# Performance work log

Measured on AMD Instinct MI355X. Metric: run time of the kernel, lower is better.

Reference implementation:

```python
import jax, jax.numpy as jnp
import numpy as np

BETA = 1.0  # lagr_softmax default inverse temperature

def setup_inputs() -> dict:
    key = jax.random.key(0)
    ks = jax.random.split(key, 5)
    B, Tq, Tk, Eq, Ek, E, H = 2, 2048, 2048, 1024, 1024, 1024, 16
    s = lambda d: 1.0 / np.sqrt(d)
    return {
        "gq": jax.random.normal(ks[0], (B, Tq, Eq), jnp.float32),
        "gk": jax.random.normal(ks[1], (B, Tk, Ek), jnp.float32),
        "WQ": jax.random.normal(ks[2], (E, Eq), jnp.float32) * s(Eq),
        "WK": jax.random.normal(ks[3], (E, Ek), jnp.float32) * s(Ek),
        "Wmix": jax.random.normal(ks[4], (1, H), jnp.float32) * s(H),
    }

def reference(gq, gk, WQ, WK, Wmix):
    B, Tq, _ = gq.shape
    H = Wmix.shape[1]
    E = WQ.shape[0]
    D = E // H
    # Linear projections (bias=False): x @ W.T
    q = (gq @ WQ.T).reshape(B, Tq, H, D)          # (B,Tq,H,D)
    k = (gk @ WK.T).reshape(B, -1, H, D)          # (B,Tk,H,D)
    # scores q @ k^T per head: (B,H,Tq,Tk)
    a = jnp.einsum('bqhd,bkhd->bhqk', q, k)
    # mix_heads: Linear(n_heads -> 1) applied over head axis
    a = jnp.einsum('bhqk,h->bqk', a, Wmix[0])     # (B,Tq,Tk)
    # lagr_softmax: (1/beta) * logsumexp(beta * a, dim=-1)
    out = jax.nn.logsumexp(BETA * a, axis=-1) / BETA  # (B,Tq)
    return out[:, None, :]                        # (B,1,Tq) matching torch shape
```

## Files before the change

### kernel.cpp

```cpp
#include <hip/hip_runtime.h>
#include <hip/hip_bf16.h>
#include <math.h>

#define B_    2
#define TQ    2048
#define TK    2048
#define E_    1024
#define MTOT  4096

typedef __attribute__((ext_vector_type(8))) short bf16x8;
typedef __attribute__((ext_vector_type(4))) float f32x4;

__device__ __forceinline__ unsigned short f2bf(float x) {
  unsigned int u = __float_as_uint(x);
  u += 0x7fff + ((u >> 16) & 1);
  return (unsigned short)(u >> 16);
}

__device__ __forceinline__ void load_lds16(const void* g, void* l) {
  __builtin_amdgcn_global_load_lds(
      (const __attribute__((address_space(1))) unsigned int*)g,
      (__attribute__((address_space(3))) unsigned int*)l, 16, 0, 0);
}

#define BARRIER() do { asm volatile("" ::: "memory"); __builtin_amdgcn_s_barrier(); asm volatile("" ::: "memory"); } while (0)
#define WAIT_VM6()   asm volatile("s_waitcnt vmcnt(6)" ::: "memory")
#define WAIT_VM0()   asm volatile("s_waitcnt vmcnt(0)" ::: "memory")


__device__ __forceinline__ void stage_A(const unsigned short* gsrc, unsigned short* lds,
                                        int tid, int kt) {
  const int r  = tid >> 3;
  const int c8 = ((tid & 7) ^ (r & 7)) * 8;
  const unsigned short* g = gsrc + (size_t)r * E_ + (size_t)kt * 64 + c8;
  unsigned short* l = lds + tid * 8;
#pragma unroll
  for (int i = 0; i < 4; ++i)
    load_lds16(g + (size_t)(64 * i) * E_, l + 4096 * i);
}
__device__ __forceinline__ void stage_B(const unsigned short* gsrc, unsigned short* lds,
                                        int tid, int kt) {
  const int r  = tid >> 3;
  const int c8 = ((tid & 7) ^ (r & 7)) * 8;
  const unsigned short* g = gsrc + (size_t)r * E_ + (size_t)kt * 64 + c8;
  unsigned short* l = lds + tid * 8;
#pragma unroll
  for (int i = 0; i < 2; ++i)
    load_lds16(g + (size_t)(64 * i) * E_, l + 4096 * i);
}

#define LDS_AT(base, row, o) ((const bf16x8*)((base) + (((row) * 128 + ((o) ^ (((row) & 7) << 4))) >> 1)))

#define READ_A_ALL()                                                          \
  do {                                                                        \
    _Pragma("unroll") for (int f = 0; f < 4; ++f)                             \
      _Pragma("unroll") for (int ks = 0; ks < 2; ++ks)                        \
        a[f][ks] = *LDS_AT(Ac, wm * 64 + f * 16 + li16, ks * 64 + hi4 * 16);  \
  } while (0)

#define READ_B(g0)                                                            \
  do {                                                                        \
    _Pragma("unroll") for (int g = (g0); g < (g0) + 2; ++g)                   \
      _Pragma("unroll") for (int ks = 0; ks < 2; ++ks)                        \
        b[g][ks] = *LDS_AT(Bc, wn * 64 + g * 16 + li16, ks * 64 + hi4 * 16);  \
  } while (0)

#define MFMA_HALF(g0)                                                         \
  do {                                                                        \
    __builtin_amdgcn_s_setprio(1);                                            \
    _Pragma("unroll") for (int ks = 0; ks < 2; ++ks)                          \
      _Pragma("unroll") for (int f = 0; f < 4; ++f)                           \
        _Pragma("unroll") for (int g = (g0); g < (g0) + 2; ++g)               \
          acc[f][g] = __builtin_amdgcn_mfma_f32_16x16x32_bf16(                \
              a[f][ks], b[g][ks], acc[f][g], 0, 0, 0);                        \
    __builtin_amdgcn_s_setprio(0);                                            \
  } while (0)

#define GEMM_PIPELINE()                                                       \
  do {                                                                        \
    stage_B(Bg, Bsl[0], tid, 0); stage_A(Ag, Asl[0], tid, 0);                 \
    stage_B(Bg, Bsl[1], tid, 1); stage_A(Ag, Asl[1], tid, 1);                 \
    WAIT_VM6();                   \
    int s0 = 0, s2 = 2;                                     \
    for (int t = 0; t < 16; ++t) {                                            \
      BARRIER();                                                              \
      const unsigned short* Ac = Asl[s0];                                     \
      const unsigned short* Bc = Bsl[s0];                                     \
                                                         \
      READ_A_ALL(); READ_B(0);                                                \
      stage_B(Bg, Bsl[s2], tid, (t + 2) & 15);                                \
      MFMA_HALF(0);                                                           \
                                                        \
      READ_B(2);                                                              \
      stage_A(Ag, Asl[s2], tid, (t + 2) & 15);                                \
      MFMA_HALF(2);                                                           \
      WAIT_VM6();                                                             \
      s0 = (s0 == 2) ? 0 : s0 + 1;                                            \
      s2 = (s2 == 2) ? 0 : s2 + 1;                                            \
    }                                                                         \
  } while (0)

__global__ void prep_kernel(const float* __restrict__ gq, const float* __restrict__ gk,
                            const float* __restrict__ WQ, const float* __restrict__ WK,
                            const float* __restrict__ Wmix,
                            unsigned short* __restrict__ gqb, unsigned short* __restrict__ gkb,
                            unsigned short* __restrict__ wqb, unsigned short* __restrict__ wkb) {
  const int NGQ = (B_ * TQ * E_) / 4;
  const int NW  = (E_ * E_) / 4;
  const int total = 2 * NGQ + 2 * NW;
  for (int idx = blockIdx.x * blockDim.x + threadIdx.x; idx < total;
       idx += gridDim.x * blockDim.x) {
    const float4* src; unsigned short* dst; int local; float scale = 1.0f;
    if (idx < NGQ)            { src = (const float4*)gq; dst = gqb; local = idx; }
    else if (idx < 2 * NGQ)   { src = (const float4*)gk; dst = gkb; local = idx - NGQ; }
    else if (idx < 2*NGQ+NW)  { src = (const float4*)WQ; dst = wqb; local = idx - 2*NGQ;
                                scale = Wmix[local >> 14]; }
    else                      { src = (const float4*)WK; dst = wkb; local = idx - 2*NGQ - NW; }
    float4 v = src[local];
    ushort4 o;
    o.x = f2bf(v.x * scale); o.y = f2bf(v.y * scale);
    o.z = f2bf(v.z * scale); o.w = f2bf(v.w * scale);
    ((ushort4*)dst)[local] = o;
  }
}

__global__ __launch_bounds__(512, 2) void proj_kernel(
    const unsigned short* __restrict__ gqb, const unsigned short* __restrict__ gkb,
    const unsigned short* __restrict__ wqb, const unsigned short* __restrict__ wkb,
    unsigned short* __restrict__ qp, unsigned short* __restrict__ kp) {
  __shared__ __align__(16) unsigned short Asl[3][16384];
  __shared__ __align__(16) unsigned short Bsl[3][8192];
  const int g_  = blockIdx.x;
  const int xcd = g_ & 7, j = g_ >> 3;
  const int side = xcd >> 2, r_ = xcd & 3;
  const int mt = r_ * 4 + (j & 3);
  const int nt = j >> 2;
  const int m0 = mt * 256, n0 = nt * 128;
  const unsigned short* Ag = (side ? gkb : gqb) + (size_t)m0 * E_;
  const unsigned short* Bg = (side ? wkb : wqb) + (size_t)n0 * E_;
  unsigned short* C        = (side ? kp  : qp);
  const int tid = threadIdx.x, wave = tid >> 6, lane = tid & 63;
  const int wm = wave >> 1, wn = wave & 1, li16 = lane & 15, hi4 = lane >> 4;
  f32x4 acc[4][4] = {};
  bf16x8 a[4][2];
  bf16x8 b[4][2];
  GEMM_PIPELINE();
#pragma unroll
  for (int f = 0; f < 4; ++f)
#pragma unroll
    for (int g = 0; g < 4; ++g)
#pragma unroll
      for (int j2 = 0; j2 < 4; ++j2) {
        int row = m0 + wm * 64 + f * 16 + hi4 * 4 + j2;
        int col = n0 + wn * 64 + g * 16 + li16;
        C[(size_t)row * E_ + col] = f2bf(acc[f][g][j2]);
      }
  WAIT_VM0();
}

__global__ __launch_bounds__(512, 2) void score_lse_kernel(
    const unsigned short* __restrict__ qp, const unsigned short* __restrict__ kp,
    float2* __restrict__ partials) {
  __shared__ __align__(16) unsigned short Asl[3][16384];
  __shared__ __align__(16) unsigned short Bsl[3][8192];
  __shared__ float redM[2][256];
  __shared__ float redS[2][256];
  const int g_  = blockIdx.x;
  const int xcd = g_ & 7, j = g_ >> 3;
  const int bb = xcd >> 2, r_ = xcd & 3;
  const int qt = (r_ & 1) * 4 + (j & 3);
  const int kt = (r_ >> 1) * 8 + (j >> 2);
  const int m0 = qt * 256, n0 = kt * 128;
  const unsigned short* Ag = qp + (size_t)bb * TQ * E_ + (size_t)m0 * E_;
  const unsigned short* Bg = kp + (size_t)bb * TK * E_ + (size_t)n0 * E_;
  const int tid = threadIdx.x, wave = tid >> 6, lane = tid & 63;
  const int wm = wave >> 1, wn = wave & 1, li16 = lane & 15, hi4 = lane >> 4;
  f32x4 acc[4][4] = {};
  bf16x8 a[4][2];
  bf16x8 b[4][2];
  GEMM_PIPELINE();
#pragma unroll
  for (int f = 0; f < 4; ++f) {
#pragma unroll
    for (int j2 = 0; j2 < 4; ++j2) {
      float m = fmaxf(fmaxf(acc[f][0][j2], acc[f][1][j2]),
                      fmaxf(acc[f][2][j2], acc[f][3][j2]));
#pragma unroll
      for (int msk = 1; msk < 16; msk <<= 1) m = fmaxf(m, __shfl_xor(m, msk, 64));
      float s = 0.f;
#pragma unroll
      for (int g = 0; g < 4; ++g) s += expf(acc[f][g][j2] - m);
#pragma unroll
      for (int msk = 1; msk < 16; msk <<= 1) s += __shfl_xor(s, msk, 64);
      if (li16 == 0) {
        int row = wm * 64 + f * 16 + hi4 * 4 + j2;
        redM[wn][row] = m;
        redS[wn][row] = s;
      }
    }
  }
  __syncthreads();
  if (tid < 256) {
    float mA = redM[0][tid], mB = redM[1][tid];
    float M = fmaxf(mA, mB);
    float S = redS[0][tid] * expf(mA - M) + redS[1][tid] * expf(mB - M);
    int qrow = bb * TQ + m0 + tid;
    partials[(size_t)qrow * 16 + kt] = make_float2(M, S);
  }
}

__global__ void finalize_kernel(const float2* __restrict__ partials, float* __restrict__ out) {
  int r = blockIdx.x * blockDim.x + threadIdx.x;
  if (r >= MTOT) return;
  const float2* p = partials + (size_t)r * 16;
  float M = p[0].x;
#pragma unroll
  for (int i = 1; i < 16; ++i) M = fmaxf(M, p[i].x);
  float S = 0.f;
#pragma unroll
  for (int i = 0; i < 16; ++i) S += p[i].y * expf(p[i].x - M);
  out[r] = logf(S) + M;
}

extern "C" void kernel_launch(void* const* d_in, const int* in_sizes, int n_in,
                              void* d_out, int out_size, void* d_ws, size_t ws_size,
                              hipStream_t stream) {
  const float* gq   = (const float*)d_in[0];
  const float* gk   = (const float*)d_in[1];
  const float* WQ   = (const float*)d_in[2];
  const float* WK   = (const float*)d_in[3];
  const float* Wmix = (const float*)d_in[4];
  float* out = (float*)d_out;

  char* ws = (char*)d_ws;
  unsigned short* gqb = (unsigned short*)(ws);
  unsigned short* gkb = (unsigned short*)(ws + 8388608);
  unsigned short* wqb = (unsigned short*)(ws + 16777216);
  unsigned short* wkb = (unsigned short*)(ws + 18874368);
  unsigned short* qp  = (unsigned short*)(ws + 20971520);
  unsigned short* kp  = (unsigned short*)(ws + 29360128);
  float2* partials    = (float2*)(ws + 37748736);

  hipLaunchKernelGGL(prep_kernel, dim3(1024), dim3(256), 0, stream,
                     gq, gk, WQ, WK, Wmix, gqb, gkb, wqb, wkb);
  hipLaunchKernelGGL(proj_kernel, dim3(256), dim3(512), 0, stream,
                     gqb, gkb, wqb, wkb, qp, kp);
  hipLaunchKernelGGL(score_lse_kernel, dim3(256), dim3(512), 0, stream,
                     qp, kp, partials);
  hipLaunchKernelGGL(finalize_kernel, dim3(16), dim3(256), 0, stream,
                     partials, out);
}
```

Measured before the change: 132.0 us.

## Load A fragments directly to registers and shrink tiles to 128x128 with 256 threads

Both GEMM kernels move from 256x128 tiles with 512 threads to 128x128 tiles with 256 threads and twice as many blocks. A operands are no longer staged through LDS; each wave loads its A fragments straight from global memory into double-buffered registers one k-step ahead. Only B goes through the 3-stage LDS ring. The aim is to cut LDS traffic and capacity use and raise block count. The cost is uncoalesced-ish direct global reads of A, more register pressure, and no reuse of A across the two wn waves.

```diff
diff --git a/kernel.cpp b/kernel.cpp
--- a/kernel.cpp
+++ b/kernel.cpp
@@ -24,20 +24,9 @@
 }
 
 #define BARRIER() do { asm volatile("" ::: "memory"); __builtin_amdgcn_s_barrier(); asm volatile("" ::: "memory"); } while (0)
-#define WAIT_VM6()   asm volatile("s_waitcnt vmcnt(6)" ::: "memory")
+#define WAIT_VM12()  asm volatile("s_waitcnt vmcnt(12)" ::: "memory")
 #define WAIT_VM0()   asm volatile("s_waitcnt vmcnt(0)" ::: "memory")
 
-
-__device__ __forceinline__ void stage_A(const unsigned short* gsrc, unsigned short* lds,
-                                        int tid, int kt) {
-  const int r  = tid >> 3;
-  const int c8 = ((tid & 7) ^ (r & 7)) * 8;
-  const unsigned short* g = gsrc + (size_t)r * E_ + (size_t)kt * 64 + c8;
-  unsigned short* l = lds + tid * 8;
-#pragma unroll
-  for (int i = 0; i < 4; ++i)
-    load_lds16(g + (size_t)(64 * i) * E_, l + 4096 * i);
-}
 __device__ __forceinline__ void stage_B(const unsigned short* gsrc, unsigned short* lds,
                                         int tid, int kt) {
   const int r  = tid >> 3;
@@ -45,58 +34,62 @@
   const unsigned short* g = gsrc + (size_t)r * E_ + (size_t)kt * 64 + c8;
   unsigned short* l = lds + tid * 8;
 #pragma unroll
-  for (int i = 0; i < 2; ++i)
-    load_lds16(g + (size_t)(64 * i) * E_, l + 4096 * i);
+  for (int i = 0; i < 4; ++i)
+    load_lds16(g + (size_t)(32 * i) * E_, l + 2048 * i);
 }
 
 #define LDS_AT(base, row, o) ((const bf16x8*)((base) + (((row) * 128 + ((o) ^ (((row) & 7) << 4))) >> 1)))
 
-#define READ_A_ALL()                                                          \
+#define LOAD_A(dst, kt)                                                       \
   do {                                                                        \
     _Pragma("unroll") for (int f = 0; f < 4; ++f)                             \
       _Pragma("unroll") for (int ks = 0; ks < 2; ++ks)                        \
-        a[f][ks] = *LDS_AT(Ac, wm * 64 + f * 16 + li16, ks * 64 + hi4 * 16);  \
-  } while (0)
-
-#define READ_B(g0)                                                            \
-  do {                                                                        \
-    _Pragma("unroll") for (int g = (g0); g < (g0) + 2; ++g)                   \
+        dst[f][ks] = *(const bf16x8*)(Ag + (size_t)(wm * 64 + f * 16 + li16) * E_ \
+                                         + (size_t)(kt) * 64 + ks * 32 + hi4 * 8); \
+  } while (0)
+
+#define READ_B()                                                              \
+  do {                                                                        \
+    _Pragma("unroll") for (int g = 0; g < 4; ++g)                             \
       _Pragma("unroll") for (int ks = 0; ks < 2; ++ks)                        \
         b[g][ks] = *LDS_AT(Bc, wn * 64 + g * 16 + li16, ks * 64 + hi4 * 16);  \
   } while (0)
 
-#define MFMA_HALF(g0)                                                         \
+#define MFMA_ALL(av)                                                          \
   do {                                                                        \
     __builtin_amdgcn_s_setprio(1);                                            \
     _Pragma("unroll") for (int ks = 0; ks < 2; ++ks)                          \
       _Pragma("unroll") for (int f = 0; f < 4; ++f)                           \
-        _Pragma("unroll") for (int g = (g0); g < (g0) + 2; ++g)               \
+        _Pragma("unroll") for (int g = 0; g < 4; ++g)                         \
           acc[f][g] = __builtin_amdgcn_mfma_f32_16x16x32_bf16(                \
-              a[f][ks], b[g][ks], acc[f][g], 0, 0, 0);                        \
+              av[f][ks], b[g][ks], acc[f][g], 0, 0, 0);                       \
     __builtin_amdgcn_s_setprio(0);                                            \
   } while (0)
 
+#define HALF_STEP(acur, anext, t)                                             \
+  do {                                                                        \
+    LOAD_A(anext, ((t) + 1) & 15);                                            \
+    stage_B(Bg, Bsl[s2], tid, ((t) + 2) & 15);                                \
+    const unsigned short* Bc = Bsl[s0];                                       \
+    READ_B();                                                                 \
+    MFMA_ALL(acur);                                                           \
+    WAIT_VM12();                                                              \
+    BARRIER();                                                                \
+    s0 = (s0 == 2) ? 0 : s0 + 1;                                              \
+    s2 = (s2 == 2) ? 0 : s2 + 1;                                              \
+  } while (0)
+
 #define GEMM_PIPELINE()                                                       \
   do {                                                                        \
-    stage_B(Bg, Bsl[0], tid, 0); stage_A(Ag, Asl[0], tid, 0);                 \
-    stage_B(Bg, Bsl[1], tid, 1); stage_A(Ag, Asl[1], tid, 1);                 \
-    WAIT_VM6();                   \
-    int s0 = 0, s2 = 2;                                     \
-    for (int t = 0; t < 16; ++t) {                                            \
-      BARRIER();                                                              \
-      const unsigned short* Ac = Asl[s0];                                     \
-      const unsigned short* Bc = Bsl[s0];                                     \
-                                                         \
-      READ_A_ALL(); READ_B(0);                                                \
-      stage_B(Bg, Bsl[s2], tid, (t + 2) & 15);                                \
-      MFMA_HALF(0);                                                           \
-                                                        \
-      READ_B(2);                                                              \
-      stage_A(Ag, Asl[s2], tid, (t + 2) & 15);                                \
-      MFMA_HALF(2);                                                           \
-      WAIT_VM6();                                                             \
-      s0 = (s0 == 2) ? 0 : s0 + 1;                                            \
-      s2 = (s2 == 2) ? 0 : s2 + 1;                                            \
+    stage_B(Bg, Bsl[0], tid, 0);                                              \
+    LOAD_A(aA, 0);                                                            \
+    stage_B(Bg, Bsl[1], tid, 1);                                              \
+    WAIT_VM12();                                                              \
+    BARRIER();                                                                \
+    int s0 = 0, s2 = 2;                                                       \
+    _Pragma("unroll 1") for (int it = 0; it < 8; ++it) {                      \
+      HALF_STEP(aA, aB, 2 * it);                                              \
+      HALF_STEP(aB, aA, 2 * it + 1);                                          \
     }                                                                         \
   } while (0)
 
@@ -124,25 +117,24 @@
   }
 }
 
-__global__ __launch_bounds__(512, 2) void proj_kernel(
+__global__ __launch_bounds__(256, 2) void proj_kernel(
     const unsigned short* __restrict__ gqb, const unsigned short* __restrict__ gkb,
     const unsigned short* __restrict__ wqb, const unsigned short* __restrict__ wkb,
     unsigned short* __restrict__ qp, unsigned short* __restrict__ kp) {
-  __shared__ __align__(16) unsigned short Asl[3][16384];
   __shared__ __align__(16) unsigned short Bsl[3][8192];
   const int g_  = blockIdx.x;
   const int xcd = g_ & 7, j = g_ >> 3;
   const int side = xcd >> 2, r_ = xcd & 3;
-  const int mt = r_ * 4 + (j & 3);
-  const int nt = j >> 2;
-  const int m0 = mt * 256, n0 = nt * 128;
+  const int mt = r_ * 8 + (j & 7);
+  const int nt = j >> 3;
+  const int m0 = mt * 128, n0 = nt * 128;
   const unsigned short* Ag = (side ? gkb : gqb) + (size_t)m0 * E_;
   const unsigned short* Bg = (side ? wkb : wqb) + (size_t)n0 * E_;
   unsigned short* C        = (side ? kp  : qp);
   const int tid = threadIdx.x, wave = tid >> 6, lane = tid & 63;
   const int wm = wave >> 1, wn = wave & 1, li16 = lane & 15, hi4 = lane >> 4;
   f32x4 acc[4][4] = {};
-  bf16x8 a[4][2];
+  bf16x8 aA[4][2], aB[4][2];
   bf16x8 b[4][2];
   GEMM_PIPELINE();
 #pragma unroll
@@ -158,25 +150,24 @@
   WAIT_VM0();
 }
 
-__global__ __launch_bounds__(512, 2) void score_lse_kernel(
+__global__ __launch_bounds__(256, 2) void score_lse_kernel(
     const unsigned short* __restrict__ qp, const unsigned short* __restrict__ kp,
     float2* __restrict__ partials) {
-  __shared__ __align__(16) unsigned short Asl[3][16384];
   __shared__ __align__(16) unsigned short Bsl[3][8192];
-  __shared__ float redM[2][256];
-  __shared__ float redS[2][256];
+  __shared__ float redM[2][128];
+  __shared__ float redS[2][128];
   const int g_  = blockIdx.x;
   const int xcd = g_ & 7, j = g_ >> 3;
   const int bb = xcd >> 2, r_ = xcd & 3;
-  const int qt = (r_ & 1) * 4 + (j & 3);
-  const int kt = (r_ >> 1) * 8 + (j >> 2);
-  const int m0 = qt * 256, n0 = kt * 128;
+  const int qt = (r_ & 1) * 8 + (j & 7);
+  const int kt = (r_ >> 1) * 8 + (j >> 3);
+  const int m0 = qt * 128, n0 = kt * 128;
   const unsigned short* Ag = qp + (size_t)bb * TQ * E_ + (size_t)m0 * E_;
   const unsigned short* Bg = kp + (size_t)bb * TK * E_ + (size_t)n0 * E_;
   const int tid = threadIdx.x, wave = tid >> 6, lane = tid & 63;
   const int wm = wave >> 1, wn = wave & 1, li16 = lane & 15, hi4 = lane >> 4;
   f32x4 acc[4][4] = {};
-  bf16x8 a[4][2];
+  bf16x8 aA[4][2], aB[4][2];
   bf16x8 b[4][2];
   GEMM_PIPELINE();
 #pragma unroll
@@ -200,7 +191,7 @@
     }
   }
   __syncthreads();
-  if (tid < 256) {
+  if (tid < 128) {
     float mA = redM[0][tid], mB = redM[1][tid];
     float M = fmaxf(mA, mB);
     float S = redS[0][tid] * expf(mA - M) + redS[1][tid] * expf(mB - M);
@@ -243,9 +234,9 @@
 
   hipLaunchKernelGGL(prep_kernel, dim3(1024), dim3(256), 0, stream,
                      gq, gk, WQ, WK, Wmix, gqb, gkb, wqb, wkb);
-  hipLaunchKernelGGL(proj_kernel, dim3(256), dim3(512), 0, stream,
+  hipLaunchKernelGGL(proj_kernel, dim3(512), dim3(256), 0, stream,
                      gqb, gkb, wqb, wkb, qp, kp);
-  hipLaunchKernelGGL(score_lse_kernel, dim3(256), dim3(512), 0, stream,
+  hipLaunchKernelGGL(score_lse_kernel, dim3(512), dim3(256), 0, stream,
                      qp, kp, partials);
   hipLaunchKernelGGL(finalize_kernel, dim3(16), dim3(256), 0, stream,
                      partials, out);
```

New measurement: 175.2 us. 1.33x slower.
